# Performance work log

Measured on AMD Instinct MI355X. Metric: run time of the kernel, lower is better.

Reference implementation:

```python
import jax, jax.numpy as jnp
import numpy as np
import math

H = 1024
NH = 16
D = H // NH  # 64
EPS = 1e-5


def _layernorm(x, g, b):
    mu = jnp.mean(x, axis=-1, keepdims=True)
    var = jnp.mean(jnp.square(x - mu), axis=-1, keepdims=True)
    return (x - mu) * jax.lax.rsqrt(var + EPS) * g + b


def setup_inputs() -> dict:
    key = jax.random.key(0)
    ks = jax.random.split(key, 12)
    B, T = 2, 2048
    q = jax.random.normal(ks[0], (B, T, H), jnp.float32)
    k = jax.random.normal(ks[1], (B, T, H), jnp.float32)
    v = jax.random.normal(ks[2], (B, T, H), jnp.float32)
    pad_mask = jax.random.randint(ks[3], (B, T), 0, 2) > 0
    s = 0.02
    Wq = jax.random.normal(ks[4], (H, H), jnp.float32) * s
    Wk = jax.random.normal(ks[5], (H, H), jnp.float32) * s
    Wv = jax.random.normal(ks[6], (H, H), jnp.float32) * s
    Wo = jax.random.normal(ks[7], (H, H), jnp.float32) * s
    W1 = jax.random.normal(ks[8], (4 * H, H), jnp.float32) * s
    b1 = jnp.zeros((4 * H,), jnp.float32)
    W2 = jax.random.normal(ks[9], (H, 4 * H), jnp.float32) * s
    b2 = jnp.zeros((H,), jnp.float32)
    g1 = jnp.ones((H,), jnp.float32); be1 = jnp.zeros((H,), jnp.float32)
    g2 = jnp.ones((H,), jnp.float32); be2 = jnp.zeros((H,), jnp.float32)
    return dict(q=q, k=k, v=v, pad_mask=pad_mask, Wq=Wq, Wk=Wk, Wv=Wv, Wo=Wo,
                W1=W1, b1=b1, W2=W2, b2=b2, g1=g1, be1=be1, g2=g2, be2=be2)


def reference(q, k, v, pad_mask, Wq, Wk, Wv, Wo, W1, b1, W2, b2, g1, be1, g2, be2):
    B, Tq, _ = q.shape
    Tv = v.shape[1]
    # torch nn.Linear: x @ W.T
    Q = (q @ Wq.T).reshape(B, NH, Tq, D)  # faithful to torch .view head split
    K = (k @ Wk.T).reshape(B, NH, Tv, D)
    V = (v @ Wv.T).reshape(B, NH, Tv, D)
    logits = jnp.einsum('baih,bajh->baij', Q, K)  # [B,NH,Tq,Tv]
    neg_inf = jnp.float32(-jnp.inf)
    logits = jnp.where(pad_mask[:, None, None, :], logits, neg_inf)
    attn = jax.nn.softmax(logits / math.sqrt(D), axis=-1)
    # post-softmax query-mask multiply (custom)
    attn = attn * pad_mask[:, None, :, None].astype(attn.dtype)
    h = jnp.einsum('baij,bajh->baih', attn, V).reshape(B, Tq, H)
    h = h @ Wo.T
    h = _layernorm(q + h, g1, be1)
    ff = jax.nn.gelu(h @ W1.T + b1, approximate=False) @ W2.T + b2  # dropout = identity (eval)
    return _layernorm(h + ff, g2, be2)
```

## Files before the change

### kernel.cpp

```cpp
#include <hip/hip_runtime.h>

typedef unsigned short u16;
typedef unsigned int u32;
typedef __attribute__((ext_vector_type(8))) __bf16 bf16x8;
typedef __attribute__((ext_vector_type(4))) float f32x4;
typedef __attribute__((ext_vector_type(16))) float f32x16;
typedef __attribute__((ext_vector_type(4))) unsigned short u16x4;
typedef __attribute__((ext_vector_type(8))) unsigned short u16x8;

#define LOG2E 1.44269504088896340736f

__device__ __forceinline__ u16 f2bf(float f) {
  union { float f; unsigned u; } c; c.f = f;
  unsigned r = c.u + 0x7FFFu + ((c.u >> 16) & 1u);
  return (u16)(r >> 16);
}
__device__ __forceinline__ float bf2f(u16 h) {
  union { unsigned u; float f; } c; c.u = ((unsigned)h) << 16;
  return c.f;
}

__device__ __forceinline__ void gload_lds16(const u16* g, u16* l) {
  __builtin_amdgcn_global_load_lds((const __attribute__((address_space(1))) unsigned int*)g,
                                   (__attribute__((address_space(3))) unsigned int*)l, 16, 0, 0);
}

__global__ __launch_bounds__(256) void cvt_all(
    const float* __restrict__ s0, const float* __restrict__ s1, const float* __restrict__ s2,
    const float* __restrict__ s3, const float* __restrict__ s4, const float* __restrict__ s5,
    const float* __restrict__ s6, const float* __restrict__ s7, const float* __restrict__ s8,
    u16* __restrict__ d0, u16* __restrict__ d1, u16* __restrict__ d2,
    u16* __restrict__ d3, u16* __restrict__ d4, u16* __restrict__ d5,
    u16* __restrict__ d6, u16* __restrict__ d7, u16* __restrict__ d8) {
  int i = blockIdx.x * 256 + threadIdx.x;
  if (i >= 6291456) return;
  const float* src; u16* dst; int off;
  if (i < 3145728) {
    if (i < 1048576)      { src = s0; dst = d0; off = 0; }
    else if (i < 2097152) { src = s1; dst = d1; off = 1048576; }
    else                  { src = s2; dst = d2; off = 2097152; }
  } else if (i < 4194304) {
    if (i < 3407872)      { src = s3; dst = d3; off = 3145728; }
    else if (i < 3670016) { src = s4; dst = d4; off = 3407872; }
    else if (i < 3932160) { src = s5; dst = d5; off = 3670016; }
    else                  { src = s6; dst = d6; off = 3932160; }
  } else {
    if (i < 5242880)      { src = s7; dst = d7; off = 4194304; }
    else                  { src = s8; dst = d8; off = 5242880; }
  }
  int j = i - off;
  f32x4 v = ((const f32x4*)src)[j];
  u16x4 o;
  o[0] = f2bf(v[0]); o[1] = f2bf(v[1]); o[2] = f2bf(v[2]); o[3] = f2bf(v[3]);
  ((u16x4*)dst)[j] = o;
}

__global__ void build_masks(const void* __restrict__ pm, float* __restrict__ maskbias,
                            float* __restrict__ qmask, int n) {
  __shared__ int sflag;
  if (threadIdx.x == 0) sflag = 0;
  __syncthreads();
  const unsigned* pw = (const unsigned*)pm;
  int nwords = n / 4;
  int local = 0;
  for (int i = threadIdx.x; i < nwords; i += blockDim.x)
    if (pw[i] > 1u) local = 1;
  if (local) atomicOr(&sflag, 1);
  __syncthreads();
  bool isbool = (sflag != 0);
  for (int i = threadIdx.x; i < n; i += blockDim.x) {
    int m = isbool ? (int)((const unsigned char*)pm)[i] : ((const int*)pm)[i];
    maskbias[i] = m ? 0.0f : -2e30f;
    qmask[i]    = m ? 1.0f : 0.0f;
  }
}

template<int EPI>
__device__ __forceinline__ void gemm_core(const u16* __restrict__ A, const u16* __restrict__ Bw,
                                          const float* __restrict__ bias, u16* __restrict__ C,
                                          int N, int K, int bn, int bm, int tid) {
  __shared__ u16 As[128 * 32];
  __shared__ u16 Bs[128 * 32];
  int wave = tid >> 6, lane = tid & 63;
  int l15 = lane & 15, l4 = lane >> 4;
  int wr = (wave >> 1) * 64, wc = (wave & 1) * 64;
  int mrow0 = bm * 128, ncol0 = bn * 128;
  int srow = lane >> 2;
  int scol = (lane & 3) * 8;

  f32x4 acc[4][4];
#pragma unroll
  for (int i = 0; i < 4; i++)
#pragma unroll
    for (int j = 0; j < 4; j++) acc[i][j] = (f32x4)0.0f;

  for (int k0 = 0; k0 < K; k0 += 32) {
#pragma unroll
    for (int c = 0; c < 2; c++) {
      int q = wave * 2 + c;
      gload_lds16(A  + (size_t)(mrow0 + q * 16 + srow) * K + k0 + scol, &As[q * 512]);
      gload_lds16(Bw + (size_t)(ncol0 + q * 16 + srow) * K + k0 + scol, &Bs[q * 512]);
    }
    __syncthreads();
    bf16x8 af[4], bfr[4];
#pragma unroll
    for (int mi = 0; mi < 4; mi++) af[mi]  = *(const bf16x8*)(&As[(wr + mi * 16 + l15) * 32 + l4 * 8]);
#pragma unroll
    for (int ni = 0; ni < 4; ni++) bfr[ni] = *(const bf16x8*)(&Bs[(wc + ni * 16 + l15) * 32 + l4 * 8]);
#pragma unroll
    for (int mi = 0; mi < 4; mi++)
#pragma unroll
      for (int ni = 0; ni < 4; ni++)
        acc[mi][ni] = __builtin_amdgcn_mfma_f32_16x16x32_bf16(af[mi], bfr[ni], acc[mi][ni], 0, 0, 0);
    __syncthreads();
  }

#pragma unroll
  for (int ni = 0; ni < 4; ni++) {
    int gcol = ncol0 + wc + ni * 16 + l15;
    float bv = (EPI > 0) ? bias[gcol] : 0.0f;
#pragma unroll
    for (int mi = 0; mi < 4; mi++) {
#pragma unroll
      for (int r = 0; r < 4; r++) {
        int grow = mrow0 + wr + mi * 16 + l4 * 4 + r;
        float v = acc[mi][ni][r] + bv;
        if (EPI == 2) v = 0.5f * v * (1.0f + erff(v * 0.70710678118654752f));
        C[(size_t)grow * N + gcol] = f2bf(v);
      }
    }
  }
}

template<int EPI>
__global__ __launch_bounds__(256) void gemm_bt(const u16* __restrict__ A, const u16* __restrict__ Bw,
                                               const float* __restrict__ bias, u16* __restrict__ C,
                                               int N, int K) {
  gemm_core<EPI>(A, Bw, bias, C, N, K, blockIdx.x, blockIdx.y, threadIdx.x);
}

__global__ __launch_bounds__(256) void gemm_qkv(const u16* __restrict__ qb, const u16* __restrict__ kb,
                                                const u16* __restrict__ vb,
                                                const u16* __restrict__ wq, const u16* __restrict__ wk,
                                                const u16* __restrict__ wv,
                                                u16* __restrict__ Qo, u16* __restrict__ Ko, u16* __restrict__ Vo) {
  const u16* A; const u16* W; u16* C;
  if (blockIdx.z == 0)      { A = qb; W = wq; C = Qo; }
  else if (blockIdx.z == 1) { A = kb; W = wk; C = Ko; }
  else                      { A = vb; W = wv; C = Vo; }
  gemm_core<0>(A, W, nullptr, C, 1024, 1024, blockIdx.x, blockIdx.y, threadIdx.x);
}

__global__ __launch_bounds__(256) void transpose64(const u16* __restrict__ in, u16* __restrict__ out) {
  int bh = blockIdx.y, tb = blockIdx.x;
  __shared__ u16 tile[64 * 72];
  int tid = threadIdx.x;
#pragma unroll
  for (int it = 0; it < 2; it++) {
    int idx = it * 256 + tid;
    int r = idx >> 3, c8 = (idx & 7) * 8;
    u16x8 v = *(const u16x8*)(in + ((size_t)bh * 2048 + tb * 64 + r) * 64 + c8);
    int byte = ((r * 72 + c8) * 2) ^ (((r >> 3) & 7) << 4);
    *(u16x8*)((char*)tile + byte) = v;
  }
  __syncthreads();
#pragma unroll
  for (int it = 0; it < 2; it++) {
    int idx = it * 256 + tid;
    int d = idx >> 3, t8 = (idx & 7) * 8;
    u16x8 o;
#pragma unroll
    for (int e = 0; e < 8; e++) {
      int t = t8 + e;
      int byte = ((t * 72 + d) * 2) ^ (((t >> 3) & 7) << 4);
      o[e] = *(const u16*)((const char*)tile + byte);
    }
    *(u16x8*)(out + ((size_t)bh * 64 + d) * 2048 + tb * 64 + t8) = o;
  }
}

__global__ __launch_bounds__(256, 4) void attn4(const u16* __restrict__ Q, const u16* __restrict__ Kg,
                                                const u16* __restrict__ VT,
                                                const float* __restrict__ maskbias,
                                                u16* __restrict__ O0, u16* __restrict__ O1,
                                                float* __restrict__ Ms, float* __restrict__ Ss) {
  const int T = 2048;
  int bh = blockIdx.x;
  int qt = blockIdx.y;
  int sp = blockIdx.z;
  int b = bh >> 4;
  const u16* Qh = Q  + (size_t)bh * T * 64;
  const u16* Kh = Kg + (size_t)bh * T * 64;
  const u16* Vh = VT + (size_t)bh * T * 64;
  u16* Oh = (sp ? O1 : O0) + (size_t)bh * T * 64;
  const float* mb = maskbias + b * T + sp * 1024;
  int tid = threadIdx.x, w = tid >> 6, l = tid & 63;
  int q32 = l & 31, h = l >> 5;
  int qbase = qt * 128 + w * 32;
  const float C = 0.125f * LOG2E;

  __shared__ u16 Ks[2][4096];
  __shared__ u16 Vs[2][4096];

  bf16x8 qf[4];
#pragma unroll
  for (int dc = 0; dc < 4; dc++)
    qf[dc] = *(const bf16x8*)(Qh + (size_t)(qbase + q32) * 64 + dc * 16 + h * 8);

  int rl = l >> 3, ob = (l & 7) * 16;
  int osw = ob ^ (rl << 4);
  int r0 = w * 16 + rl, r1 = w * 16 + 8 + rl;
  const u16* pK0 = Kh + (size_t)(sp * 1024 + r0) * 64 + (osw >> 1);
  const u16* pK1 = Kh + (size_t)(sp * 1024 + r1) * 64 + (osw >> 1);
  const u16* pV0 = Vh + (size_t)r0 * 2048 + sp * 1024 + (osw >> 1);
  const u16* pV1 = Vh + (size_t)r1 * 2048 + sp * 1024 + (osw >> 1);
  u16* dK0 = &Ks[0][0] + (w * 16) * 64;
  u16* dK1 = &Ks[0][0] + (w * 16 + 8) * 64;
  u16* dV0 = &Vs[0][0] + (w * 16) * 64;
  u16* dV1 = &Vs[0][0] + (w * 16 + 8) * 64;

  auto stage = [&](int buf) {
    gload_lds16(pK0, dK0 + buf * 4096);
    gload_lds16(pK1, dK1 + buf * 4096);
    gload_lds16(pV0, dV0 + buf * 4096);
    gload_lds16(pV1, dV1 + buf * 4096);
    pK0 += 4096; pK1 += 4096; pV0 += 64; pV1 += 64;
  };

  f32x16 acc[2];
  acc[0] = (f32x16)0.0f; acc[1] = (f32x16)0.0f;
  float m_ = -3e30f, s_ = 0.0f;

  int swz = (q32 & 7) << 4;

  stage(0);
  for (int t = 0; t < 16; t++) {
    int cur = t & 1;
    __syncthreads();
    if (t < 15) stage(cur ^ 1);
    const char* ksb = (const char*)(&Ks[0][0] + cur * 4096);
    const char* vsb = (const char*)(&Vs[0][0] + cur * 4096);

    bf16x8 kf[2][4];
#pragma unroll
    for (int kvc = 0; kvc < 2; kvc++)
#pragma unroll
      for (int dc = 0; dc < 4; dc++)
        kf[kvc][dc] = *(const bf16x8*)(ksb + (kvc * 32 + q32) * 128 + ((dc * 32 + h * 16) ^ swz));

    f32x16 st[2];
    st[0] = (f32x16)0.0f; st[1] = (f32x16)0.0f;
#pragma unroll
    for (int kvc = 0; kvc < 2; kvc++)
#pragma unroll
      for (int dc = 0; dc < 4; dc++)
        st[kvc] = __builtin_amdgcn_mfma_f32_32x32x16_bf16(kf[kvc][dc], qf[dc], st[kvc], 0, 0, 0);

    float p[32];
    float pmax = -3e30f;
#pragma unroll
    for (int kvc = 0; kvc < 2; kvc++) {
#pragma unroll
      for (int g = 0; g < 4; g++) {
        f32x4 mv = *(const f32x4*)(mb + t * 64 + kvc * 32 + g * 8 + h * 4);
#pragma unroll
        for (int r = 0; r < 4; r++) {
          float val = st[kvc][g * 4 + r] * C + mv[r];
          p[kvc * 16 + g * 4 + r] = val;
          pmax = fmaxf(pmax, val);
        }
      }
    }
    pmax = fmaxf(pmax, __shfl_xor(pmax, 32));

    if (__any(pmax - m_ > 8.0f)) {
      float mnew = fmaxf(m_, pmax);
      float fsc = __builtin_amdgcn_exp2f(m_ - mnew);
      s_ *= fsc;
      m_ = mnew;
#pragma unroll
      for (int g = 0; g < 4; g++)
#pragma unroll
        for (int r = 0; r < 4; r++) {
          float f = __shfl(fsc, g * 8 + h * 4 + r);
          acc[0][g * 4 + r] *= f;
          acc[1][g * 4 + r] *= f;
        }
    }

    float rsum = 0.0f;
    u32 wds[16];
#pragma unroll
    for (int i = 0; i < 16; i++) {
      float a = __builtin_amdgcn_exp2f(p[2 * i] - m_);
      float bq = __builtin_amdgcn_exp2f(p[2 * i + 1] - m_);
      rsum += a + bq;
      union { __bf16 h2[2]; u32 u; } cv;
      cv.h2[0] = (__bf16)a; cv.h2[1] = (__bf16)bq;
      wds[i] = cv.u;
    }
    rsum += __shfl_xor(rsum, 32);
    s_ += rsum;

#pragma unroll
    for (int kvc = 0; kvc < 2; kvc++) {
      int bse = kvc * 8;
      u32 sw0 = __shfl_xor(wds[bse + 0], 32), sw1 = __shfl_xor(wds[bse + 1], 32);
      u32 sw2 = __shfl_xor(wds[bse + 2], 32), sw3 = __shfl_xor(wds[bse + 3], 32);
      u32 sw4 = __shfl_xor(wds[bse + 4], 32), sw5 = __shfl_xor(wds[bse + 5], 32);
      u32 sw6 = __shfl_xor(wds[bse + 6], 32), sw7 = __shfl_xor(wds[bse + 7], 32);
      union { u32 u[4]; bf16x8 v; } pa0, pa1;
      pa0.u[0] = h ? sw2 : wds[bse + 0];
      pa0.u[1] = h ? sw3 : wds[bse + 1];
      pa0.u[2] = h ? wds[bse + 2] : sw0;
      pa0.u[3] = h ? wds[bse + 3] : sw1;
      pa1.u[0] = h ? sw6 : wds[bse + 4];
      pa1.u[1] = h ? sw7 : wds[bse + 5];
      pa1.u[2] = h ? wds[bse + 6] : sw4;
      pa1.u[3] = h ? wds[bse + 7] : sw5;
#pragma unroll
      for (int cl = 0; cl < 2; cl++) {
        bf16x8 pa = cl ? pa1.v : pa0.v;
        int cg = kvc * 2 + cl;
#pragma unroll
        for (int dblk = 0; dblk < 2; dblk++) {
          bf16x8 vf = *(const bf16x8*)(vsb + (dblk * 32 + q32) * 128 + ((cg * 32 + h * 16) ^ swz));
          acc[dblk] = __builtin_amdgcn_mfma_f32_32x32x16_bf16(pa, vf, acc[dblk], 0, 0, 0);
        }
      }
    }
  }

#pragma unroll
  for (int g = 0; g < 4; g++) {
#pragma unroll
    for (int r = 0; r < 4; r++) {
      int row = g * 8 + h * 4 + r;
#pragma unroll
      for (int dblk = 0; dblk < 2; dblk++)
        Oh[(size_t)(qbase + row) * 64 + dblk * 32 + q32] = f2bf(acc[dblk][g * 4 + r]);
    }
  }
  if (h == 0) {
    int ro = sp * 65536 + bh * 2048 + qbase + q32;
    Ms[ro] = m_;
    Ss[ro] = s_;
  }
}

__global__ __launch_bounds__(256) void attn_combine(const u16* __restrict__ O0, const u16* __restrict__ O1,
                                                    const float* __restrict__ Ms, const float* __restrict__ Ss,
                                                    const float* __restrict__ qmaskf, u16* __restrict__ out) {
  int idx = blockIdx.x * 256 + threadIdx.x;
  int row = idx >> 3;
  int d8 = (idx & 7) * 8;
  int bh = row >> 11, r = row & 2047, b = bh >> 4;
  float m0 = Ms[row], m1 = Ms[65536 + row];
  float mstar = fmaxf(m0, m1);
  float w0 = __builtin_amdgcn_exp2f(m0 - mstar);
  float w1 = __builtin_amdgcn_exp2f(m1 - mstar);
  float den = w0 * Ss[row] + w1 * Ss[65536 + row];
  float scale = qmaskf[b * 2048 + r] / den;
  size_t base = (size_t)row * 64 + d8;
  u16x8 a0 = *(const u16x8*)(O0 + base);
  u16x8 a1 = *(const u16x8*)(O1 + base);
  u16x8 o;
#pragma unroll
  for (int e = 0; e < 8; e++)
    o[e] = f2bf((w0 * bf2f(a0[e]) + w1 * bf2f(a1[e])) * scale);
  *(u16x8*)(out + base) = o;
}

template<int A_F32, int OUT_F32>
__global__ __launch_bounds__(256) void add_ln(const void* __restrict__ Ap, const u16* __restrict__ Bp,
                                              const float* __restrict__ g, const float* __restrict__ be,
                                              void* __restrict__ outp) {
  int row = blockIdx.x, tid = threadIdx.x;
  int lane = tid & 63, wave = tid >> 6;
  float x[4];
  if (A_F32) {
    f32x4 a = ((const f32x4*)((const float*)Ap + (size_t)row * 1024))[tid];
    u16x4 bu = ((const u16x4*)(Bp + (size_t)row * 1024))[tid];
#pragma unroll
    for (int j = 0; j < 4; j++) x[j] = a[j] + bf2f(bu[j]);
  } else {
    u16x4 au = ((const u16x4*)((const u16*)Ap + (size_t)row * 1024))[tid];
    u16x4 bu = ((const u16x4*)(Bp + (size_t)row * 1024))[tid];
#pragma unroll
    for (int j = 0; j < 4; j++) x[j] = bf2f(au[j]) + bf2f(bu[j]);
  }
  float s = x[0] + x[1] + x[2] + x[3];
  float q = x[0] * x[0] + x[1] * x[1] + x[2] * x[2] + x[3] * x[3];
#pragma unroll
  for (int m = 1; m < 64; m <<= 1) { s += __shfl_xor(s, m); q += __shfl_xor(q, m); }
  __shared__ float rs[4], rq[4];
  if (lane == 0) { rs[wave] = s; rq[wave] = q; }
  __syncthreads();
  float S = rs[0] + rs[1] + rs[2] + rs[3];
  float Qq = rq[0] + rq[1] + rq[2] + rq[3];
  float mean = S * (1.0f / 1024.0f);
  float var = Qq * (1.0f / 1024.0f) - mean * mean;
  float rstd = rsqrtf(var + 1e-5f);
  if (OUT_F32) {
    f32x4 y;
#pragma unroll
    for (int j = 0; j < 4; j++) { int col = tid * 4 + j; y[j] = (x[j] - mean) * rstd * g[col] + be[col]; }
    ((f32x4*)((float*)outp + (size_t)row * 1024))[tid] = y;
  } else {
    u16x4 y;
#pragma unroll
    for (int j = 0; j < 4; j++) { int col = tid * 4 + j; y[j] = f2bf((x[j] - mean) * rstd * g[col] + be[col]); }
    ((u16x4*)((u16*)outp + (size_t)row * 1024))[tid] = y;
  }
}

extern "C" void kernel_launch(void* const* d_in, const int* in_sizes, int n_in,
                              void* d_out, int out_size, void* d_ws, size_t ws_size,
                              hipStream_t stream) {
  const float* q   = (const float*)d_in[0];
  const float* k   = (const float*)d_in[1];
  const float* v   = (const float*)d_in[2];
  const void*  pad = d_in[3];
  const float* Wq  = (const float*)d_in[4];
  const float* Wk  = (const float*)d_in[5];
  const float* Wv  = (const float*)d_in[6];
  const float* Wo  = (const float*)d_in[7];
  const float* W1  = (const float*)d_in[8];
  const float* b1  = (const float*)d_in[9];
  const float* W2  = (const float*)d_in[10];
  const float* b2  = (const float*)d_in[11];
  const float* g1  = (const float*)d_in[12];
  const float* be1 = (const float*)d_in[13];
  const float* g2  = (const float*)d_in[14];
  const float* be2 = (const float*)d_in[15];
  float* out = (float*)d_out;
  char* ws = (char*)d_ws;
  const size_t MB = 1u << 20;

  u16* wq_b = (u16*)(ws + 0 * MB);
  u16* wk_b = (u16*)(ws + 2 * MB);
  u16* wv_b = (u16*)(ws + 4 * MB);
  u16* wo_b = (u16*)(ws + 6 * MB);
  u16* w1_b = (u16*)(ws + 8 * MB);
  u16* w2_b = (u16*)(ws + 16 * MB);
  u16* qb   = (u16*)(ws + 24 * MB);
  u16* kb   = (u16*)(ws + 32 * MB);
  u16* vb   = (u16*)(ws + 40 * MB);
  u16* Qb   = (u16*)(ws + 48 * MB);
  u16* Kb   = (u16*)(ws + 56 * MB);
  u16* Vb   = (u16*)(ws + 64 * MB);
  u16* VTb  = (u16*)(ws + 72 * MB);
  u16* hatt = (u16*)(ws + 80 * MB);
  u16* atto = (u16*)(ws + 88 * MB);
  u16* Op0  = (u16*)(ws + 24 * MB);
  u16* Op1  = (u16*)(ws + 32 * MB);
  float* Ms = (float*)(ws + 88 * MB);
  float* Ss = (float*)(ws + 89 * MB);
  u16* h1b  = (u16*)(ws + 24 * MB);
  u16* ff1  = (u16*)(ws + 32 * MB);
  u16* ff2  = (u16*)(ws + 64 * MB);
  float* maskbias = (float*)(ws + 96 * MB);
  float* qmaskf   = (float*)(ws + 96 * MB + 16384);

  build_masks<<<1, 256, 0, stream>>>(pad, maskbias, qmaskf, in_sizes[3]);

  cvt_all<<<24576, 256, 0, stream>>>(q, k, v, Wq, Wk, Wv, Wo, W1, W2,
                                     qb, kb, vb, wq_b, wk_b, wv_b, wo_b, w1_b, w2_b);

  gemm_qkv<<<dim3(8, 32, 3), 256, 0, stream>>>(qb, kb, vb, wq_b, wk_b, wv_b, Qb, Kb, Vb);

  transpose64<<<dim3(32, 32), 256, 0, stream>>>(Vb, VTb);

  attn4<<<dim3(32, 16, 2), 256, 0, stream>>>(Qb, Kb, VTb, maskbias, Op0, Op1, Ms, Ss);

  attn_combine<<<2048, 256, 0, stream>>>(Op0, Op1, Ms, Ss, qmaskf, hatt);

  gemm_bt<0><<<dim3(8, 32), 256, 0, stream>>>(hatt, wo_b, nullptr, atto, 1024, 1024);

  add_ln<1, 0><<<4096, 256, 0, stream>>>(q, atto, g1, be1, h1b);

  gemm_bt<2><<<dim3(32, 32), 256, 0, stream>>>(h1b, w1_b, b1, ff1, 4096, 1024);
  gemm_bt<1><<<dim3(8, 32), 256, 0, stream>>>(ff1, w2_b, b2, ff2, 1024, 4096);

  add_ln<0, 1><<<4096, 256, 0, stream>>>(h1b, ff2, g2, be2, out);
}
```

Baseline: 333.7 us.

## Split-K the Wo and FF2 GEMMs and fuse partial reduction into LayerNorm

The output-projection and second FFN GEMMs now run as split-K launches (2 and 4 K-slices) that each write bf16 partial products. The add+LayerNorm kernels are generalized to sum the partials, plus the bias for FF2, before normalizing. This raises the block count of these N=1024 GEMMs from 256 to 512/1024 to fill the GPU better. The trade-off is extra partial-buffer memory traffic and bf16 rounding of each partial.

New measurement: 313.1 us. 6.2% less time.

```diff
diff --git a/kernel.cpp b/kernel.cpp
--- a/kernel.cpp
+++ b/kernel.cpp
@@ -78,7 +78,7 @@
 template<int EPI>
 __device__ __forceinline__ void gemm_core(const u16* __restrict__ A, const u16* __restrict__ Bw,
                                           const float* __restrict__ bias, u16* __restrict__ C,
-                                          int N, int K, int bn, int bm, int tid) {
+                                          int N, int Kstride, int Klen, int bn, int bm, int tid) {
   __shared__ u16 As[128 * 32];
   __shared__ u16 Bs[128 * 32];
   int wave = tid >> 6, lane = tid & 63;
@@ -94,12 +94,12 @@
 #pragma unroll
     for (int j = 0; j < 4; j++) acc[i][j] = (f32x4)0.0f;
 
-  for (int k0 = 0; k0 < K; k0 += 32) {
+  for (int k0 = 0; k0 < Klen; k0 += 32) {
 #pragma unroll
     for (int c = 0; c < 2; c++) {
       int q = wave * 2 + c;
-      gload_lds16(A  + (size_t)(mrow0 + q * 16 + srow) * K + k0 + scol, &As[q * 512]);
-      gload_lds16(Bw + (size_t)(ncol0 + q * 16 + srow) * K + k0 + scol, &Bs[q * 512]);
+      gload_lds16(A  + (size_t)(mrow0 + q * 16 + srow) * Kstride + k0 + scol, &As[q * 512]);
+      gload_lds16(Bw + (size_t)(ncol0 + q * 16 + srow) * Kstride + k0 + scol, &Bs[q * 512]);
     }
     __syncthreads();
     bf16x8 af[4], bfr[4];
@@ -136,7 +136,15 @@
 __global__ __launch_bounds__(256) void gemm_bt(const u16* __restrict__ A, const u16* __restrict__ Bw,
                                                const float* __restrict__ bias, u16* __restrict__ C,
                                                int N, int K) {
-  gemm_core<EPI>(A, Bw, bias, C, N, K, blockIdx.x, blockIdx.y, threadIdx.x);
+  gemm_core<EPI>(A, Bw, bias, C, N, K, K, blockIdx.x, blockIdx.y, threadIdx.x);
+}
+
+__global__ __launch_bounds__(256) void gemm_splitk(const u16* __restrict__ A, const u16* __restrict__ Bw,
+                                                   u16* __restrict__ P, int N, int Kstride, int Kc) {
+  int z = blockIdx.z;
+  size_t M = (size_t)gridDim.y * 128;
+  gemm_core<0>(A + (size_t)z * Kc, Bw + (size_t)z * Kc, nullptr,
+               P + (size_t)z * M * N, N, Kstride, Kc, blockIdx.x, blockIdx.y, threadIdx.x);
 }
 
 __global__ __launch_bounds__(256) void gemm_qkv(const u16* __restrict__ qb, const u16* __restrict__ kb,
@@ -148,7 +156,7 @@
   if (blockIdx.z == 0)      { A = qb; W = wq; C = Qo; }
   else if (blockIdx.z == 1) { A = kb; W = wk; C = Ko; }
   else                      { A = vb; W = wv; C = Vo; }
-  gemm_core<0>(A, W, nullptr, C, 1024, 1024, blockIdx.x, blockIdx.y, threadIdx.x);
+  gemm_core<0>(A, W, nullptr, C, 1024, 1024, 1024, blockIdx.x, blockIdx.y, threadIdx.x);
 }
 
 __global__ __launch_bounds__(256) void transpose64(const u16* __restrict__ in, u16* __restrict__ out) {
@@ -371,23 +379,50 @@
   *(u16x8*)(out + base) = o;
 }
 
-template<int A_F32, int OUT_F32>
-__global__ __launch_bounds__(256) void add_ln(const void* __restrict__ Ap, const u16* __restrict__ Bp,
-                                              const float* __restrict__ g, const float* __restrict__ be,
-                                              void* __restrict__ outp) {
+template<int NP, int A_F32, int ADD_BIAS, int OUT_F32>
+__global__ __launch_bounds__(256) void add_ln_multi(const void* __restrict__ Ap,
+                                                    const u16* __restrict__ P0, const u16* __restrict__ P1,
+                                                    const u16* __restrict__ P2, const u16* __restrict__ P3,
+                                                    const float* __restrict__ bias,
+                                                    const float* __restrict__ g, const float* __restrict__ be,
+                                                    void* __restrict__ outp) {
   int row = blockIdx.x, tid = threadIdx.x;
   int lane = tid & 63, wave = tid >> 6;
+  size_t rb = (size_t)row * 1024;
   float x[4];
   if (A_F32) {
-    f32x4 a = ((const f32x4*)((const float*)Ap + (size_t)row * 1024))[tid];
-    u16x4 bu = ((const u16x4*)(Bp + (size_t)row * 1024))[tid];
-#pragma unroll
-    for (int j = 0; j < 4; j++) x[j] = a[j] + bf2f(bu[j]);
+    f32x4 a = ((const f32x4*)((const float*)Ap + rb))[tid];
+#pragma unroll
+    for (int j = 0; j < 4; j++) x[j] = a[j];
   } else {
-    u16x4 au = ((const u16x4*)((const u16*)Ap + (size_t)row * 1024))[tid];
-    u16x4 bu = ((const u16x4*)(Bp + (size_t)row * 1024))[tid];
-#pragma unroll
-    for (int j = 0; j < 4; j++) x[j] = bf2f(au[j]) + bf2f(bu[j]);
+    u16x4 au = ((const u16x4*)((const u16*)Ap + rb))[tid];
+#pragma unroll
+    for (int j = 0; j < 4; j++) x[j] = bf2f(au[j]);
+  }
+  {
+    u16x4 p = ((const u16x4*)(P0 + rb))[tid];
+#pragma unroll
+    for (int j = 0; j < 4; j++) x[j] += bf2f(p[j]);
+  }
+  if (NP > 1) {
+    u16x4 p = ((const u16x4*)(P1 + rb))[tid];
+#pragma unroll
+    for (int j = 0; j < 4; j++) x[j] += bf2f(p[j]);
+  }
+  if (NP > 2) {
+    u16x4 p = ((const u16x4*)(P2 + rb))[tid];
+#pragma unroll
+    for (int j = 0; j < 4; j++) x[j] += bf2f(p[j]);
+  }
+  if (NP > 3) {
+    u16x4 p = ((const u16x4*)(P3 + rb))[tid];
+#pragma unroll
+    for (int j = 0; j < 4; j++) x[j] += bf2f(p[j]);
+  }
+  if (ADD_BIAS) {
+    f32x4 bv = ((const f32x4*)bias)[tid];
+#pragma unroll
+    for (int j = 0; j < 4; j++) x[j] += bv[j];
   }
   float s = x[0] + x[1] + x[2] + x[3];
   float q = x[0] * x[0] + x[1] * x[1] + x[2] * x[2] + x[3] * x[3];
@@ -405,12 +440,12 @@
     f32x4 y;
 #pragma unroll
     for (int j = 0; j < 4; j++) { int col = tid * 4 + j; y[j] = (x[j] - mean) * rstd * g[col] + be[col]; }
-    ((f32x4*)((float*)outp + (size_t)row * 1024))[tid] = y;
+    ((f32x4*)((float*)outp + rb))[tid] = y;
   } else {
     u16x4 y;
 #pragma unroll
     for (int j = 0; j < 4; j++) { int col = tid * 4 + j; y[j] = f2bf((x[j] - mean) * rstd * g[col] + be[col]); }
-    ((u16x4*)((u16*)outp + (size_t)row * 1024))[tid] = y;
+    ((u16x4*)((u16*)outp + rb))[tid] = y;
   }
 }
 
@@ -451,14 +486,14 @@
   u16* Vb   = (u16*)(ws + 64 * MB);
   u16* VTb  = (u16*)(ws + 72 * MB);
   u16* hatt = (u16*)(ws + 80 * MB);
-  u16* atto = (u16*)(ws + 88 * MB);
   u16* Op0  = (u16*)(ws + 24 * MB);
   u16* Op1  = (u16*)(ws + 32 * MB);
   float* Ms = (float*)(ws + 88 * MB);
   float* Ss = (float*)(ws + 89 * MB);
+  u16* WP   = (u16*)(ws + 40 * MB);
   u16* h1b  = (u16*)(ws + 24 * MB);
   u16* ff1  = (u16*)(ws + 32 * MB);
-  u16* ff2  = (u16*)(ws + 64 * MB);
+  u16* Fp   = (u16*)(ws + 64 * MB);
   float* maskbias = (float*)(ws + 96 * MB);
   float* qmaskf   = (float*)(ws + 96 * MB + 16384);
 
@@ -475,12 +510,15 @@
 
   attn_combine<<<2048, 256, 0, stream>>>(Op0, Op1, Ms, Ss, qmaskf, hatt);
 
-  gemm_bt<0><<<dim3(8, 32), 256, 0, stream>>>(hatt, wo_b, nullptr, atto, 1024, 1024);
-
-  add_ln<1, 0><<<4096, 256, 0, stream>>>(q, atto, g1, be1, h1b);
+  gemm_splitk<<<dim3(8, 32, 2), 256, 0, stream>>>(hatt, wo_b, WP, 1024, 1024, 512);
+
+  add_ln_multi<2, 1, 0, 0><<<4096, 256, 0, stream>>>(q, WP, WP + 4194304, nullptr, nullptr,
+                                                     nullptr, g1, be1, h1b);
 
   gemm_bt<2><<<dim3(32, 32), 256, 0, stream>>>(h1b, w1_b, b1, ff1, 4096, 1024);
-  gemm_bt<1><<<dim3(8, 32), 256, 0, stream>>>(ff1, w2_b, b2, ff2, 1024, 4096);
-
-  add_ln<0, 1><<<4096, 256, 0, stream>>>(h1b, ff2, g2, be2, out);
-}
+
+  gemm_splitk<<<dim3(8, 32, 4), 256, 0, stream>>>(ff1, w2_b, Fp, 1024, 4096, 1024);
+
+  add_ln_multi<4, 0, 1, 1><<<4096, 256, 0, stream>>>(h1b, Fp, Fp + 4194304, Fp + 2 * 4194304,
+                                                     Fp + 3 * 4194304, b2, g2, be2, out);
+}
```
